# Kernel tuning notes

Hardware: AMD Instinct MI355X
Metric: run time of the kernel (lower is better)

## Reference

```python
import jax, jax.numpy as jnp
import numpy as np

B, D, O, K = 8192, 256, 256, 16


def setup_inputs() -> dict:
    key = jax.random.key(0)
    k1, k2, k3, k4 = jax.random.split(key, 4)
    x = jax.random.normal(k1, (B, D), dtype=jnp.float32)
    # learned params
    values = jax.random.uniform(k2, (O, D, K), dtype=jnp.float32, minval=-0.05, maxval=0.05)
    skip_w = jax.random.normal(k3, (O, D), dtype=jnp.float32) * (1.0 / np.sqrt(D))
    skip_b = jax.random.uniform(k4, (O,), dtype=jnp.float32, minval=-1.0, maxval=1.0) / np.sqrt(D)
    # fixed buffer (non-trainable)
    grid = jnp.linspace(-1.0, 1.0, K).astype(jnp.float32)
    return {"x": x, "values": values, "skip_w": skip_w, "skip_b": skip_b, "grid": grid}


def reference(x, values, skip_w, skip_b, grid):
    # x: [B, D]; values: [O, D, K]; grid: [K]
    num_knots = grid.shape[0]
    xc = jnp.clip(x, -1.0, 1.0)
    # torch.bucketize(x, grid) (right=False) == searchsorted side='left'
    right = jnp.searchsorted(grid, xc, side="left")            # [B, D]
    left = jnp.clip(right - 1, 0, num_knots - 2)               # [B, D]
    right = left + 1
    g0 = grid[left]
    g1 = grid[right]
    w = (xc - g0) / (g1 - g0 + 1e-12)                          # [B, D]
    # sparse linear-interp coefficients over knots: 2 nonzeros per (b, d)
    coeff = (1.0 - w)[..., None] * jax.nn.one_hot(left, num_knots, dtype=xc.dtype) \
          + w[..., None] * jax.nn.one_hot(right, num_knots, dtype=xc.dtype)  # [B, D, K]
    # y[b,o] = sum_d sum_k coeff[b,d,k] * values[o,d,k]  (== per-dim gather+interp+accumulate)
    y = jnp.einsum("bdk,odk->bo", coeff, values)
    y = y + xc @ skip_w.T + skip_b
    return y
```

## Files before the change

### kernel.cpp

```cpp
#include <hip/hip_runtime.h>
#include <hip/hip_bf16.h>
#include <stdint.h>


#define D_DIM  256
#define O_DIM  256
#define BM     64
#define BN     128
#define BK     64
#define KS     4
#define ITERS  16
#define NTHR   256

typedef __attribute__((ext_vector_type(8))) short bf16x8;
typedef __attribute__((ext_vector_type(4))) float f32x4;

__global__ __launch_bounds__(256) void kan_prep(
    const float* __restrict__ values,
    const float* __restrict__ skip_w,
    const float* __restrict__ gknots,
    unsigned short* __restrict__ Vp)
{
    int tid = blockIdx.x * blockDim.x + threadIdx.x;
    int e = tid * 8;
    int o = e >> 12;
    int kflat = e & 4095;
    float sw = skip_w[(o << 8) | (kflat >> 4)];
    int kmod = kflat & 15;

    const float4* vp4 = reinterpret_cast<const float4*>(values + e);
    float4 v0 = vp4[0], v1 = vp4[1];
    float f[8] = {v0.x, v0.y, v0.z, v0.w, v1.x, v1.y, v1.z, v1.w};
    unsigned int w[4];
#pragma unroll
    for (int j = 0; j < 4; ++j) {
        float2 ab;
        ab.x = f[2*j]     + gknots[kmod + 2*j]     * sw;
        ab.y = f[2*j + 1] + gknots[kmod + 2*j + 1] * sw;
        __hip_bfloat162 p2 = __float22bfloat162_rn(ab);
        __builtin_memcpy(&w[j], &p2, 4);
    }
    size_t c = (size_t)(kflat >> 3) * 256 + (size_t)o;
    *reinterpret_cast<uint4*>(Vp + c * 8) = make_uint4(w[0], w[1], w[2], w[3]);
}

__global__ __launch_bounds__(NTHR, 4) void kan_gemm(
    const float* __restrict__ x,
    const unsigned short* __restrict__ Vp,
    float* __restrict__ part,
    float* __restrict__ out)
{
    __shared__ unsigned short As[2][BM * BK];

    const int t    = threadIdx.x;
    const int lane = t & 63;
    const int wid  = t >> 6;
    const int l15  = lane & 15;
    const int lhi  = lane >> 4;

    const int bid = (int)blockIdx.x;
    const int ks  = bid & 3;
    const int nt  = (bid >> 2) & 1;
    const int mt  = bid >> 3;
    const int bm0 = mt * BM;
    const int nc0 = nt * BN;
    const size_t kc0 = (size_t)ks * 128;

    const int ar = t >> 2;
    const int dg = t & 3;
    const float* xp = x + (size_t)(bm0 + ar) * D_DIM + ks * 64 + dg;

    char* arow[2] = { (char*)&As[0][0] + ar * 128, (char*)&As[1][0] + ar * 128 };
    const int cs0 = ((2 * dg)     ^ (ar & 7)) * 16;
    const int cs1 = ((2 * dg + 1) ^ (ar & 7)) * 16;

    auto stageA = [&](int buf, float xv) {
        float xc = fminf(1.f, fmaxf(-1.f, xv));
        float tt = (xc + 1.f) * 7.5f;
        int li = (int)tt;
        li = li > 14 ? 14 : li;
        float w1 = tt - (float)li;
        float2 cw; cw.x = 1.f - w1; cw.y = w1;
        __hip_bfloat162 p2 = __float22bfloat162_rn(cw);
        unsigned int pk;
        __builtin_memcpy(&pk, &p2, 4);
        unsigned long long w64 = (unsigned long long)pk << ((li & 1) * 16);
        unsigned int lo = (unsigned int)w64;
        unsigned int hi = (unsigned int)(w64 >> 32);
        int jl = li >> 1;
        unsigned int wd[8];
#pragma unroll
        for (int j = 0; j < 8; ++j)
            wd[j] = (j == jl) ? lo : ((j == jl + 1) ? hi : 0u);
        char* a = arow[buf];
        *reinterpret_cast<uint4*>(a + cs0) = make_uint4(wd[0], wd[1], wd[2], wd[3]);
        *reinterpret_cast<uint4*>(a + cs1) = make_uint4(wd[4], wd[5], wd[6], wd[7]);
    };

    #define LOADB(BG, KT)                                                      \
        {                                                                      \
            const unsigned short* _b = Vp + (kc0 + (size_t)(KT) * 8) * 2048;   \
            _Pragma("unroll")                                                  \
            for (int kh = 0; kh < 2; ++kh)                                     \
                _Pragma("unroll")                                              \
                for (int ni = 0; ni < 2; ++ni) {                               \
                    int n = nc0 + wid * 32 + ni * 16 + l15;                    \
                    BG[kh * 2 + ni] = *reinterpret_cast<const bf16x8*>(        \
                        _b + ((size_t)((kh * 4 + lhi) * 256 + n)) * 8);        \
                }                                                              \
        }

    int abyte[4], a7[4];
#pragma unroll
    for (int mi = 0; mi < 4; ++mi) {
        int m = mi * 16 + l15;
        abyte[mi] = m * 128;
        a7[mi] = m & 7;
    }

    f32x4 acc[4][2] = {};
    bf16x8 bgA[4], bgB[4];

    float x1 = xp[0];
    LOADB(bgA, 0);
    stageA(0, x1);
    float xn = xp[4];
    asm volatile("s_waitcnt lgkmcnt(0)" ::: "memory");
    __builtin_amdgcn_s_barrier();
    __builtin_amdgcn_sched_barrier(0);

    #define ITERBODY(KT, CUR, BGC, BGN)                                       \
        {                                                                     \
            const bool last = (KT) == ITERS - 1;                              \
            if (!last) LOADB(BGN, (KT) + 1);                                  \
            const char* Ab = (const char*)&As[CUR][0];                        \
            bf16x8 af[4][2];                                                  \
            _Pragma("unroll")                                                 \
            for (int kh = 0; kh < 2; ++kh) {                                  \
                int k8 = kh * 4 + lhi;                                        \
                _Pragma("unroll")                                             \
                for (int mi = 0; mi < 4; ++mi)                                \
                    af[mi][kh] = *reinterpret_cast<const bf16x8*>(            \
                        Ab + abyte[mi] + ((k8 ^ a7[mi]) << 4));               \
            }                                                                 \
            if (!last) {                                                      \
                stageA((CUR) ^ 1, xn);                                        \
                if ((KT) + 2 < ITERS) xn = xp[((KT) + 2) * 4];                \
            }                                                                 \
            __builtin_amdgcn_s_setprio(1);                                    \
            _Pragma("unroll")                                                 \
            for (int mi = 0; mi < 4; ++mi)                                    \
                _Pragma("unroll")                                             \
                for (int ni = 0; ni < 2; ++ni)                                \
                    _Pragma("unroll")                                         \
                    for (int kh = 0; kh < 2; ++kh)                            \
                        acc[mi][ni] = __builtin_amdgcn_mfma_f32_16x16x32_bf16(\
                            af[mi][kh], BGC[kh * 2 + ni], acc[mi][ni], 0,0,0);\
            __builtin_amdgcn_s_setprio(0);                                    \
            if (!last) {                                                      \
                asm volatile("s_waitcnt lgkmcnt(0)" ::: "memory");            \
                __builtin_amdgcn_s_barrier();                                 \
                __builtin_amdgcn_sched_barrier(0);                            \
            }                                                                 \
        }

    for (int t2 = 0; t2 < ITERS / 2; ++t2) {
        ITERBODY(2 * t2,     0, bgA, bgB);
        ITERBODY(2 * t2 + 1, 1, bgB, bgA);
    }
    #undef ITERBODY
    #undef LOADB

    float* dst = (ks == 0) ? out : part + (size_t)(ks - 1) * (8192 * 256);
#pragma unroll
    for (int ni = 0; ni < 2; ++ni) {
        int col = nc0 + wid * 32 + ni * 16 + l15;
#pragma unroll
        for (int mi = 0; mi < 4; ++mi) {
            f32x4 v = acc[mi][ni];
            int row0 = bm0 + mi * 16 + lhi * 4;
#pragma unroll
            for (int r = 0; r < 4; ++r)
                dst[(size_t)(row0 + r) * O_DIM + col] = v[r];
        }
    }
}

__global__ __launch_bounds__(256) void kan_reduce(
    const float* __restrict__ part,
    const float* __restrict__ skip_b,
    float* __restrict__ out)
{
    size_t i4 = (size_t)blockIdx.x * 256 + threadIdx.x;
    size_t e = i4 * 4;
    f32x4 s = *reinterpret_cast<const f32x4*>(out + e);
    s += *reinterpret_cast<const f32x4*>(&skip_b[e & 255]);
    s += *reinterpret_cast<const f32x4*>(part + e);
    s += *reinterpret_cast<const f32x4*>(part + (size_t)8192 * 256 + e);
    s += *reinterpret_cast<const f32x4*>(part + (size_t)2 * 8192 * 256 + e);
    *reinterpret_cast<f32x4*>(out + e) = s;
}

__global__ __launch_bounds__(256) void kan_naive(
    const float* __restrict__ x,
    const unsigned short* __restrict__ Vp,
    const float* __restrict__ skip_b,
    float* __restrict__ out)
{
    int b = blockIdx.x, o = threadIdx.x;
    float acc = skip_b[o];
    for (int d = 0; d < 256; ++d) {
        float xc = fminf(1.f, fmaxf(-1.f, x[(size_t)b * 256 + d]));
        float tt = (xc + 1.f) * 7.5f;
        int li = (int)tt; li = li > 14 ? 14 : li;
        float w1 = tt - (float)li;
        int k0 = d * 16 + li;
        unsigned short u0 = Vp[((size_t)(k0 >> 3) * 256 + o) * 8 + (k0 & 7)];
        int k1 = k0 + 1;
        unsigned short u1 = Vp[((size_t)(k1 >> 3) * 256 + o) * 8 + (k1 & 7)];
        float f0 = __uint_as_float((unsigned)u0 << 16);
        float f1 = __uint_as_float((unsigned)u1 << 16);
        acc += (1.f - w1) * f0 + w1 * f1;
    }
    out[(size_t)b * 256 + o] = acc;
}

extern "C" void kernel_launch(void* const* d_in, const int* in_sizes, int n_in,
                              void* d_out, int out_size, void* d_ws, size_t ws_size,
                              hipStream_t stream) {
    const float* x      = (const float*)d_in[0];
    const float* values = (const float*)d_in[1];
    const float* skip_w = (const float*)d_in[2];
    const float* skip_b = (const float*)d_in[3];
    const float* gknots = (const float*)d_in[4];
    float* out = (float*)d_out;
    (void)in_sizes; (void)n_in; (void)out_size;

    unsigned short* Vp = (unsigned short*)d_ws;
    float* part = (float*)((char*)d_ws + 2u * 1024 * 1024);

    kan_prep<<<dim3(512), dim3(256), 0, stream>>>(values, skip_w, gknots, Vp);

    const size_t need = 2u * 1024 * 1024
                      + (size_t)3 * 8192 * 256 * sizeof(float);
    if (ws_size >= need) {
        kan_gemm<<<dim3(1024), dim3(NTHR), 0, stream>>>(x, Vp, part, out);
        kan_reduce<<<dim3(2048), dim3(256), 0, stream>>>(part, skip_b, out);
    } else {
        kan_naive<<<dim3(8192), dim3(256), 0, stream>>>(x, Vp, skip_b, out);
    }
}
```

Before: 41.07 us.

## Drop split-K partials and reduce kernel; use 64x64 tiles over full K

Removes the 4-way split-K and the separate reduction kernel. Each block now computes a 64x64 output tile over the full K=4096 (64 iterations), with a 2x2 wave layout, and adds skip_b in the epilogue. Block index mapping is swizzled for L2 locality. This avoids writing and re-reading about 24MB of fp32 partials and one launch. In exchange it runs fewer blocks (512) with a longer serial K loop, lower occupancy bounds and less reuse per block; setprio is also removed.

```diff
diff --git a/kernel.cpp b/kernel.cpp
--- a/kernel.cpp
+++ b/kernel.cpp
@@ -6,10 +6,8 @@
 #define D_DIM  256
 #define O_DIM  256
 #define BM     64
-#define BN     128
-#define BK     64
-#define KS     4
-#define ITERS  16
+#define BN     64
+#define ITERS  64
 #define NTHR   256
 
 typedef __attribute__((ext_vector_type(8))) short bf16x8;
@@ -44,31 +42,31 @@
     *reinterpret_cast<uint4*>(Vp + c * 8) = make_uint4(w[0], w[1], w[2], w[3]);
 }
 
-__global__ __launch_bounds__(NTHR, 4) void kan_gemm(
+__global__ __launch_bounds__(NTHR, 2) void kan_gemm(
     const float* __restrict__ x,
     const unsigned short* __restrict__ Vp,
-    float* __restrict__ part,
+    const float* __restrict__ skip_b,
     float* __restrict__ out)
 {
-    __shared__ unsigned short As[2][BM * BK];
+    __shared__ unsigned short As[2][BM * 64];
 
     const int t    = threadIdx.x;
     const int lane = t & 63;
     const int wid  = t >> 6;
+    const int wr   = wid >> 1;
+    const int wc   = wid & 1;
     const int l15  = lane & 15;
     const int lhi  = lane >> 4;
 
-    const int bid = (int)blockIdx.x;
-    const int ks  = bid & 3;
-    const int nt  = (bid >> 2) & 1;
-    const int mt  = bid >> 3;
+    const int l   = (int)blockIdx.x;
+    const int nt  = (l >> 3) & 3;
+    const int mt  = (l & 7) | ((l >> 5) << 3);
     const int bm0 = mt * BM;
     const int nc0 = nt * BN;
-    const size_t kc0 = (size_t)ks * 128;
 
     const int ar = t >> 2;
     const int dg = t & 3;
-    const float* xp = x + (size_t)(bm0 + ar) * D_DIM + ks * 64 + dg;
+    const float* xp = x + (size_t)(bm0 + ar) * D_DIM + dg;
 
     char* arow[2] = { (char*)&As[0][0] + ar * 128, (char*)&As[1][0] + ar * 128 };
     const int cs0 = ((2 * dg)     ^ (ar & 7)) * 16;
@@ -99,26 +97,26 @@
 
     #define LOADB(BG, KT)                                                      \
         {                                                                      \
-            const unsigned short* _b = Vp + (kc0 + (size_t)(KT) * 8) * 2048;   \
+            const unsigned short* _b = Vp + (size_t)(KT) * 8 * 2048;           \
             _Pragma("unroll")                                                  \
             for (int kh = 0; kh < 2; ++kh)                                     \
                 _Pragma("unroll")                                              \
                 for (int ni = 0; ni < 2; ++ni) {                               \
-                    int n = nc0 + wid * 32 + ni * 16 + l15;                    \
+                    int n = nc0 + wc * 32 + ni * 16 + l15;                     \
                     BG[kh * 2 + ni] = *reinterpret_cast<const bf16x8*>(        \
                         _b + ((size_t)((kh * 4 + lhi) * 256 + n)) * 8);        \
                 }                                                              \
         }
 
-    int abyte[4], a7[4];
-#pragma unroll
-    for (int mi = 0; mi < 4; ++mi) {
-        int m = mi * 16 + l15;
+    int abyte[2], a7[2];
+#pragma unroll
+    for (int mi = 0; mi < 2; ++mi) {
+        int m = wr * 32 + mi * 16 + l15;
         abyte[mi] = m * 128;
         a7[mi] = m & 7;
     }
 
-    f32x4 acc[4][2] = {};
+    f32x4 acc[2][2] = {};
     bf16x8 bgA[4], bgB[4];
 
     float x1 = xp[0];
@@ -134,12 +132,12 @@
             const bool last = (KT) == ITERS - 1;                              \
             if (!last) LOADB(BGN, (KT) + 1);                                  \
             const char* Ab = (const char*)&As[CUR][0];                        \
-            bf16x8 af[4][2];                                                  \
+            bf16x8 af[2][2];                                                  \
             _Pragma("unroll")                                                 \
             for (int kh = 0; kh < 2; ++kh) {                                  \
                 int k8 = kh * 4 + lhi;                                        \
                 _Pragma("unroll")                                             \
-                for (int mi = 0; mi < 4; ++mi)                                \
+                for (int mi = 0; mi < 2; ++mi)                                \
                     af[mi][kh] = *reinterpret_cast<const bf16x8*>(            \
                         Ab + abyte[mi] + ((k8 ^ a7[mi]) << 4));               \
             }                                                                 \
@@ -147,16 +145,14 @@
                 stageA((CUR) ^ 1, xn);                                        \
                 if ((KT) + 2 < ITERS) xn = xp[((KT) + 2) * 4];                \
             }                                                                 \
-            __builtin_amdgcn_s_setprio(1);                                    \
             _Pragma("unroll")                                                 \
-            for (int mi = 0; mi < 4; ++mi)                                    \
+            for (int mi = 0; mi < 2; ++mi)                                    \
                 _Pragma("unroll")                                             \
                 for (int ni = 0; ni < 2; ++ni)                                \
                     _Pragma("unroll")                                         \
                     for (int kh = 0; kh < 2; ++kh)                            \
                         acc[mi][ni] = __builtin_amdgcn_mfma_f32_16x16x32_bf16(\
                             af[mi][kh], BGC[kh * 2 + ni], acc[mi][ni], 0,0,0);\
-            __builtin_amdgcn_s_setprio(0);                                    \
             if (!last) {                                                      \
                 asm volatile("s_waitcnt lgkmcnt(0)" ::: "memory");            \
                 __builtin_amdgcn_s_barrier();                                 \
@@ -171,34 +167,19 @@
     #undef ITERBODY
     #undef LOADB
 
-    float* dst = (ks == 0) ? out : part + (size_t)(ks - 1) * (8192 * 256);
 #pragma unroll
     for (int ni = 0; ni < 2; ++ni) {
-        int col = nc0 + wid * 32 + ni * 16 + l15;
-#pragma unroll
-        for (int mi = 0; mi < 4; ++mi) {
+        int col = nc0 + wc * 32 + ni * 16 + l15;
+        float sb = skip_b[col];
+#pragma unroll
+        for (int mi = 0; mi < 2; ++mi) {
             f32x4 v = acc[mi][ni];
-            int row0 = bm0 + mi * 16 + lhi * 4;
+            int row0 = bm0 + wr * 32 + mi * 16 + lhi * 4;
 #pragma unroll
             for (int r = 0; r < 4; ++r)
-                dst[(size_t)(row0 + r) * O_DIM + col] = v[r];
+                out[(size_t)(row0 + r) * O_DIM + col] = v[r] + sb;
         }
     }
-}
-
-__global__ __launch_bounds__(256) void kan_reduce(
-    const float* __restrict__ part,
-    const float* __restrict__ skip_b,
-    float* __restrict__ out)
-{
-    size_t i4 = (size_t)blockIdx.x * 256 + threadIdx.x;
-    size_t e = i4 * 4;
-    f32x4 s = *reinterpret_cast<const f32x4*>(out + e);
-    s += *reinterpret_cast<const f32x4*>(&skip_b[e & 255]);
-    s += *reinterpret_cast<const f32x4*>(part + e);
-    s += *reinterpret_cast<const f32x4*>(part + (size_t)8192 * 256 + e);
-    s += *reinterpret_cast<const f32x4*>(part + (size_t)2 * 8192 * 256 + e);
-    *reinterpret_cast<f32x4*>(out + e) = s;
 }
 
 __global__ __launch_bounds__(256) void kan_naive(
@@ -237,15 +218,11 @@
     (void)in_sizes; (void)n_in; (void)out_size;
 
     unsigned short* Vp = (unsigned short*)d_ws;
-    float* part = (float*)((char*)d_ws + 2u * 1024 * 1024);
 
     kan_prep<<<dim3(512), dim3(256), 0, stream>>>(values, skip_w, gknots, Vp);
 
-    const size_t need = 2u * 1024 * 1024
-                      + (size_t)3 * 8192 * 256 * sizeof(float);
-    if (ws_size >= need) {
-        kan_gemm<<<dim3(1024), dim3(NTHR), 0, stream>>>(x, Vp, part, out);
-        kan_reduce<<<dim3(2048), dim3(256), 0, stream>>>(part, skip_b, out);
+    if (ws_size >= 2u * 1024 * 1024) {
+        kan_gemm<<<dim3(512), dim3(NTHR), 0, stream>>>(x, Vp, skip_b, out);
     } else {
         kan_naive<<<dim3(8192), dim3(256), 0, stream>>>(x, Vp, skip_b, out);
     }
```

After: 40.82 us. Within noise of the previous version (-0.6%).
